# Kernel optimization log

Hardware: AMD Instinct MI355X
Metric: run time of the kernel (lower is better)

## Reference

```python
import jax, jax.numpy as jnp
import numpy as np

# dims: batch, encoder frames, encoder dim, pred-net hidden, joint dim, vocab (blank = V)
B, T, ENC, H, J, V = 32, 64, 1024, 320, 320, 1024
BLANK = V
MAXSYM = 2            # max_symbols_per_step
S = T * MAXSYM        # upper bound on loop-labels iterations (<= MAXSYM steps per frame due to force-blank)


def setup_inputs() -> dict:
    key = jax.random.key(0)
    ks = jax.random.split(key, 10)
    s = 0.05
    return {
        "x": jax.random.normal(ks[0], (B, T, ENC), jnp.float32),
        "out_len": jax.random.randint(ks[1], (B,), T // 2, T + 1, dtype=jnp.int32),
        "W_enc": jax.random.normal(ks[2], (ENC, J), jnp.float32) * s,
        "b_enc": jnp.zeros((J,), jnp.float32),
        "Emb": jax.random.normal(ks[3], (V, H), jnp.float32) * s,
        "W_ih": jax.random.normal(ks[4], (H, 4 * H), jnp.float32) * s,
        "W_hh": jax.random.normal(ks[5], (H, 4 * H), jnp.float32) * s,
        "b_lstm": jnp.zeros((4 * H,), jnp.float32),
        "W_pred": jax.random.normal(ks[6], (H, J), jnp.float32) * s,
        "b_pred": jnp.zeros((J,), jnp.float32),
        "W_out": jax.random.normal(ks[7], (J, V + 1), jnp.float32) * s,
        "b_out": jnp.zeros((V + 1,), jnp.float32),
    }


def _lstm_step(emb, h, c, W_ih, W_hh, b):
    g = emb @ W_ih + h @ W_hh + b
    i, f, gg, o = jnp.split(g, 4, axis=-1)
    c2 = jax.nn.sigmoid(f) * c + jax.nn.sigmoid(i) * jnp.tanh(gg)
    h2 = jax.nn.sigmoid(o) * jnp.tanh(c2)
    return h2, c2


def reference(x, out_len, W_enc, b_enc, Emb, W_ih, W_hh, b_lstm, W_pred, b_pred, W_out, b_out):
    # project_encoder once (as in the torch module)
    x_proj = x @ W_enc + b_enc                      # [B, T, J]
    # SOS step: zero embedding, zero LSTM state (decoder.predict(None, None))
    z = jnp.zeros((B, H), x.dtype)
    h0, c0 = _lstm_step(z, z, z, W_ih, W_hh, b_lstm)
    dec0 = h0 @ W_pred + b_pred                     # project_prednet

    def step(carry, _):
        time, symbols, h, c, dec = carry
        enc_t = jnp.take_along_axis(x_proj, time[:, None, None].astype(jnp.int32), axis=1)[:, 0]  # [B, J]
        logits = jax.nn.relu(enc_t + dec) @ W_out + b_out  # joint_after_projection, [B, V+1]
        scores = logits.max(-1)
        labels = jnp.argmax(logits, -1)
        active = time < out_len
        emit = active & (labels != BLANK)
        # prediction-network step for elements that emitted a non-blank label
        emb = Emb[jnp.where(emit, labels, 0)]
        h2, c2 = _lstm_step(emb, h, c, W_ih, W_hh, b_lstm)
        dec2 = h2 @ W_pred + b_pred
        m = emit[:, None]
        h = jnp.where(m, h2, h)
        c = jnp.where(m, c2, c)
        dec = jnp.where(m, dec2, dec)
        sym2 = jnp.where(emit, symbols + 1, jnp.zeros_like(symbols))
        force = emit & (sym2 >= MAXSYM)             # force blank after max_symbols on one frame
        advance = (active & ~emit) | force          # blank (or forced blank) advances time
        time2 = time + advance.astype(time.dtype)
        sym2 = jnp.where(advance, jnp.zeros_like(sym2), sym2)
        out = (jnp.where(emit, labels, BLANK).astype(jnp.int32),
               jnp.where(active, scores, jnp.zeros_like(scores)),
               time.astype(jnp.int32),
               emit)
        return (time2, sym2, h, c, dec), out

    init = (jnp.zeros((B,), jnp.int32), jnp.zeros((B,), jnp.int32), h0, c0, dec0)
    _, (lab, sc, tm, em) = jax.lax.scan(step, init, None, length=S)
    lengths = em.astype(jnp.int32).sum(0)
    # lab/sc/tm: [S, B] alignment-style records (BLANK filler when nothing emitted);
    # lengths: number of emitted (non-blank) labels per utterance -> equals batched_hyps contents.
    return lab, sc, tm, lengths
```

## Files before the change

kernel.cpp:

```cpp
#include <hip/hip_runtime.h>
#include <math.h>

typedef unsigned long long ull;

constexpr int Bn = 32, Tn = 64, Hn = 320, Jn = 320, Vn = 1024, Sn = 128;
constexpr int G4n = 1280, VP1 = 1025, WO4S = 1028;

constexpr int OFF_XP  = 0;
constexpr int OFF_G   = OFF_XP + Bn*Tn*Jn;
constexpr int OFF_WO4 = OFF_G + Vn*G4n;
constexpr int OFF_WH4 = OFF_WO4 + 80*WO4S*4;
constexpr int OFF_WP4 = OFF_WH4 + 80*G4n*4;
constexpr int OFF_CB  = OFF_WP4 + 80*Jn*4;
constexpr int OFF_DEC = OFF_CB + 2*Bn*Hn;
constexpr int OFF_GB  = OFF_DEC + 2*Bn*Jn;
constexpr int OFF_PB  = OFF_GB + 2*Bn*G4n;
constexpr int OFF_REC = OFF_PB + 2*Bn*8*1028;

__device__ __forceinline__ float sigmf(float x) { return 1.0f / (1.0f + expf(-x)); }

__device__ __forceinline__ ull pack_key(float v, int idx) {
    unsigned u = __float_as_uint(v);
    u = (u & 0x80000000u) ? ~u : (u | 0x80000000u);
    return ((ull)u << 32) | (unsigned)(0x7FFFFFFF - idx);
}
__device__ __forceinline__ float key_val(ull k) {
    unsigned u = (unsigned)(k >> 32);
    return __uint_as_float((u & 0x80000000u) ? (u & 0x7FFFFFFFu) : ~u);
}
__device__ __forceinline__ int key_idx(ull k) { return 0x7FFFFFFF - (int)(k & 0xFFFFFFFFu); }

__device__ __forceinline__ void gemm_tile128(const float* __restrict__ A,
                                             const float* __restrict__ Bm,
                                             const float* __restrict__ bias,
                                             float* __restrict__ C,
                                             int N, int K, int bx, int by,
                                             float (*As)[132], float (*Bs)[65]) {
    const int tx = threadIdx.x & 15, ty = threadIdx.x >> 4;
    const int n0 = bx * 64, m0 = by * 128;
    float acc[8][4] = {};
    for (int k0 = 0; k0 < K; k0 += 16) {
        for (int i = threadIdx.x; i < 2048; i += 256) {
            int mm = i >> 4, kk = i & 15;
            As[kk][mm] = A[(size_t)(m0 + mm) * K + k0 + kk];
        }
        for (int i = threadIdx.x; i < 1024; i += 256) {
            int kk2 = i >> 6, nn = i & 63;
            Bs[kk2][nn] = Bm[(size_t)(k0 + kk2) * N + n0 + nn];
        }
        __syncthreads();
#pragma unroll
        for (int kk = 0; kk < 16; ++kk) {
            float av[8], bv[4];
#pragma unroll
            for (int r = 0; r < 8; ++r) av[r] = As[kk][ty * 8 + r];
#pragma unroll
            for (int r = 0; r < 4; ++r) bv[r] = Bs[kk][tx * 4 + r];
#pragma unroll
            for (int i2 = 0; i2 < 8; ++i2)
#pragma unroll
                for (int j2 = 0; j2 < 4; ++j2) acc[i2][j2] += av[i2] * bv[j2];
        }
        __syncthreads();
    }
#pragma unroll
    for (int i2 = 0; i2 < 8; ++i2)
#pragma unroll
        for (int j2 = 0; j2 < 4; ++j2)
            C[(size_t)(m0 + ty * 8 + i2) * N + n0 + tx * 4 + j2] =
                acc[i2][j2] + bias[n0 + tx * 4 + j2];
}

__global__ __launch_bounds__(256) void preamble(
    const float* __restrict__ x, const float* __restrict__ W_enc,
    const float* __restrict__ b_enc, const float* __restrict__ Emb,
    const float* __restrict__ W_ih, const float* __restrict__ b_lstm,
    const float* __restrict__ W_hh, const float* __restrict__ W_pred,
    const float* __restrict__ W_out,
    float* __restrict__ xp, float* __restrict__ Gm,
    float* __restrict__ Wo4, float* __restrict__ Wh4, float* __restrict__ Wp4) {
    __shared__ float As[16][132];
    __shared__ float Bs[16][65];
    const int blk = blockIdx.x;
    if (blk < 80) {
        gemm_tile128(x, W_enc, b_enc, xp, Jn, 1024, blk % 5, blk / 5, As, Bs);
    } else if (blk < 240) {
        const int t = blk - 80;
        gemm_tile128(Emb, W_ih, b_lstm, Gm, G4n, Hn, t % 20, t / 20, As, Bs);
    } else if (blk < 320) {
        const int k4 = blk - 240;
        for (int c = threadIdx.x; c < VP1; c += 256) {
            float4 v;
            v.x = W_out[(k4 * 4 + 0) * VP1 + c];
            v.y = W_out[(k4 * 4 + 1) * VP1 + c];
            v.z = W_out[(k4 * 4 + 2) * VP1 + c];
            v.w = W_out[(k4 * 4 + 3) * VP1 + c];
            ((float4*)Wo4)[(size_t)k4 * WO4S + c] = v;
        }
    } else if (blk < 400) {
        const int k4 = blk - 320;
        for (int c = threadIdx.x; c < G4n; c += 256) {
            float4 v;
            v.x = W_hh[(k4 * 4 + 0) * G4n + c];
            v.y = W_hh[(k4 * 4 + 1) * G4n + c];
            v.z = W_hh[(k4 * 4 + 2) * G4n + c];
            v.w = W_hh[(k4 * 4 + 3) * G4n + c];
            ((float4*)Wh4)[(size_t)k4 * G4n + c] = v;
        }
    } else {
        const int k4 = blk - 400;
        for (int c = threadIdx.x; c < Jn; c += 256) {
            float4 v;
            v.x = W_pred[(k4 * 4 + 0) * Jn + c];
            v.y = W_pred[(k4 * 4 + 1) * Jn + c];
            v.z = W_pred[(k4 * 4 + 2) * Jn + c];
            v.w = W_pred[(k4 * 4 + 3) * Jn + c];
            ((float4*)Wp4)[(size_t)k4 * Jn + c] = v;
        }
    }
}

__global__ __launch_bounds__(320, 1) void rnnt_step(
    const float* __restrict__ xp, const float* __restrict__ Gm,
    const float* __restrict__ Wo4, const float* __restrict__ Wh4,
    const float* __restrict__ Wp4,
    const float* __restrict__ b_out, const float* __restrict__ b_lstm,
    const float* __restrict__ b_pred, const int* __restrict__ out_len,
    float* __restrict__ cb, float* __restrict__ db, float* __restrict__ gb,
    float* __restrict__ pb, int* __restrict__ rec, float* __restrict__ out,
    int L) {
    __shared__ __align__(16) float h_s[Hn];
    __shared__ __align__(16) float f_s[48];
    __shared__ float dec_s[40];
    __shared__ ull wk_s[5];

    const int w = blockIdx.x, tid = threadIdx.x;
    const int b = w & 31, m = w >> 5;
    const int ol = out_len[b];
    const float4* Wo4f = (const float4*)Wo4;
    const float4* Wh4f = (const float4*)Wh4;
    const float4* Wp4f = (const float4*)Wp4;
    const float4* h4 = (const float4*)h_s;

    int tnew, genN;
    bool doDec;
    if (L == 0) {
        float c0 = sigmf(b_lstm[tid]) * tanhf(b_lstm[2 * Hn + tid]);
        float h0 = sigmf(b_lstm[3 * Hn + tid]) * tanhf(c0);
        h_s[tid] = h0;
        int lc = tid - m * 40;
        if (lc >= 0 && lc < 40) cb[b * Hn + tid] = c0;
        if (m == 0 && tid == 0) {
            int* rn = rec + b * 4;
            rn[0] = 0; rn[1] = 0; rn[2] = 0;
        }
        tnew = 0; genN = 0; doDec = true;
        __syncthreads();
    } else {
        const int* rp = rec + ((L - 1) & 1) * Bn * 4 + b * 4;
        const int told = rp[0], sold = rp[1], len = rp[2];
        if (told >= ol) {
            if (m == 0 && tid == 0) {
                out[(L - 1) * Bn + b] = 1024.0f;
                out[Sn * Bn + (L - 1) * Bn + b] = 0.0f;
                out[2 * Sn * Bn + (L - 1) * Bn + b] = (float)told;
                int* rn = rec + (L & 1) * Bn * 4 + b * 4;
                rn[0] = told; rn[1] = 0; rn[2] = len;
                if (L == Sn) out[3 * Sn * Bn + b] = (float)len;
            }
            return;
        }
        const float* gq = gb + (size_t)((len & 1) * Bn + b) * G4n;
        const float* cv = cb + (size_t)((len & 1) * Bn + b) * Hn;
        float g0 = gq[tid], g1 = gq[Hn + tid], g2 = gq[2 * Hn + tid], g3 = gq[3 * Hn + tid];
        float crv = cv[tid];
        asm volatile("" ::: "memory");
        const float4* pp4 = (const float4*)(pb + (size_t)(((L - 1) & 1) * Bn + b) * 8 * 1028);
        ull key = 0;
        if (tid < 257) {
            float4 sv = make_float4(0.f, 0.f, 0.f, 0.f);
#pragma unroll
            for (int mm = 0; mm < 8; ++mm) {
                float4 v = pp4[mm * 257 + tid];
                sv.x += v.x; sv.y += v.y; sv.z += v.z; sv.w += v.w;
            }
            const int c0 = tid * 4;
            key = pack_key(sv.x + b_out[c0], c0);
            if (c0 + 1 < VP1) { ull k2 = pack_key(sv.y + b_out[c0 + 1], c0 + 1); if (k2 > key) key = k2; }
            if (c0 + 2 < VP1) { ull k2 = pack_key(sv.z + b_out[c0 + 2], c0 + 2); if (k2 > key) key = k2; }
            if (c0 + 3 < VP1) { ull k2 = pack_key(sv.w + b_out[c0 + 3], c0 + 3); if (k2 > key) key = k2; }
        }
#pragma unroll
        for (int d = 1; d < 64; d <<= 1) {
            ull o = __shfl_xor(key, d, 64);
            if (o > key) key = o;
        }
        if ((tid & 63) == 0) wk_s[tid >> 6] = key;
        __syncthreads();
        ull bk = wk_s[0];
#pragma unroll
        for (int i = 1; i < 5; ++i) if (wk_s[i] > bk) bk = wk_s[i];
        const int label = key_idx(bk);
        const bool emit = (label != Vn);
        int sym2 = emit ? sold + 1 : 0;
        const bool force = emit && (sym2 >= 2);
        const bool advance = (!emit) || force;
        tnew = told + (advance ? 1 : 0);
        sym2 = advance ? 0 : sym2;
        const int newlen = len + (emit ? 1 : 0);
        if (m == 0 && tid == 0) {
            out[(L - 1) * Bn + b] = emit ? (float)label : 1024.0f;
            out[Sn * Bn + (L - 1) * Bn + b] = key_val(bk);
            out[2 * Sn * Bn + (L - 1) * Bn + b] = (float)told;
            int* rn = rec + (L & 1) * Bn * 4 + b * 4;
            rn[0] = tnew; rn[1] = sym2; rn[2] = newlen;
            if (L == Sn) out[3 * Sn * Bn + b] = (float)newlen;
        }
        if (L == Sn) return;
        if (tnew >= ol) return;
        genN = newlen;
        doDec = emit;
        if (emit) {
            const float* gE = Gm + (size_t)label * G4n;
            float xi = g0 + gE[tid];
            float xf = g1 + gE[Hn + tid];
            float xg = g2 + gE[2 * Hn + tid];
            float xo = g3 + gE[3 * Hn + tid];
            float c2 = sigmf(xf) * crv + sigmf(xi) * tanhf(xg);
            float h2 = sigmf(xo) * tanhf(c2);
            h_s[tid] = h2;
            int lc = tid - m * 40;
            if (lc >= 0 && lc < 40)
                cb[(size_t)((newlen & 1) * Bn + b) * Hn + tid] = c2;
        } else {
            if (tid < 40)
                dec_s[tid] = db[(size_t)((len & 1) * Bn + b) * Jn + m * 40 + tid];
        }
        __syncthreads();
    }
    if (doDec) {
        if (tid < 160) {
            const int c = m * 160 + tid;
            float ax = 0.f, ay = 0.f, az = 0.f, aw = 0.f;
#pragma unroll 20
            for (int k4 = 0; k4 < 80; ++k4) {
                float4 wv = Wh4f[(size_t)k4 * G4n + c];
                float4 hv = h4[k4];
                ax += wv.x * hv.x; ay += wv.y * hv.y;
                az += wv.z * hv.z; aw += wv.w * hv.w;
            }
            gb[(size_t)((genN & 1) * Bn + b) * G4n + c] = ax + ay + az + aw;
        } else if (tid < 200) {
            const int lc = tid - 160;
            const int c = m * 40 + lc;
            float ax = 0.f, ay = 0.f, az = 0.f, aw = 0.f;
#pragma unroll 20
            for (int k4 = 0; k4 < 80; ++k4) {
                float4 wv = Wp4f[(size_t)k4 * Jn + c];
                float4 hv = h4[k4];
                ax += wv.x * hv.x; ay += wv.y * hv.y;
                az += wv.z * hv.z; aw += wv.w * hv.w;
            }
            float d = b_pred[c] + ax + ay + az + aw;
            dec_s[lc] = d;
            db[(size_t)((genN & 1) * Bn + b) * Jn + c] = d;
        }
        __syncthreads();
    }
    if (tid < 40) {
        const int tc = tnew < (Tn - 1) ? tnew : (Tn - 1);
        f_s[tid] = fmaxf(xp[(size_t)(b * Tn + tc) * Jn + m * 40 + tid] + dec_s[tid], 0.0f);
    }
    __syncthreads();
    {
        const float4* f4 = (const float4*)f_s;
        float4 fr[10];
#pragma unroll
        for (int j = 0; j < 10; ++j) fr[j] = f4[j];
        float* pw = pb + (size_t)((L & 1) * Bn + b) * 8 * 1028 + m * 1028;
        for (int c = tid; c < VP1; c += 320) {
            float ax = 0.f, ay = 0.f, az = 0.f, aw = 0.f;
#pragma unroll
            for (int j = 0; j < 10; ++j) {
                float4 wv = Wo4f[(size_t)(10 * m + j) * WO4S + c];
                float4 fv = fr[j];
                ax += wv.x * fv.x; ay += wv.y * fv.y;
                az += wv.z * fv.z; aw += wv.w * fv.w;
            }
            pw[c] = ax + ay + az + aw;
        }
    }
}

extern "C" void kernel_launch(void* const* d_in, const int* in_sizes, int n_in,
                              void* d_out, int out_size, void* d_ws, size_t ws_size,
                              hipStream_t stream) {
    (void)in_sizes; (void)n_in; (void)out_size; (void)ws_size;
    const float* x      = (const float*)d_in[0];
    const int*   outlen = (const int*)d_in[1];
    const float* W_enc  = (const float*)d_in[2];
    const float* b_enc  = (const float*)d_in[3];
    const float* Emb    = (const float*)d_in[4];
    const float* W_ih   = (const float*)d_in[5];
    const float* W_hh   = (const float*)d_in[6];
    const float* b_lstm = (const float*)d_in[7];
    const float* W_pred = (const float*)d_in[8];
    const float* b_pred = (const float*)d_in[9];
    const float* W_out  = (const float*)d_in[10];
    const float* b_out  = (const float*)d_in[11];

    float* ws  = (float*)d_ws;
    float* xp  = ws + OFF_XP;
    float* Gm  = ws + OFF_G;
    float* Wo4 = ws + OFF_WO4;
    float* Wh4 = ws + OFF_WH4;
    float* Wp4 = ws + OFF_WP4;
    float* cb  = ws + OFF_CB;
    float* db  = ws + OFF_DEC;
    float* gb  = ws + OFF_GB;
    float* pb  = ws + OFF_PB;
    int*   rec = (int*)(ws + OFF_REC);

    preamble<<<480, 256, 0, stream>>>(x, W_enc, b_enc, Emb, W_ih, b_lstm,
                                      W_hh, W_pred, W_out,
                                      xp, Gm, Wo4, Wh4, Wp4);

    for (int L = 0; L <= Sn; ++L)
        rnnt_step<<<256, 320, 0, stream>>>(xp, Gm, Wo4, Wh4, Wp4,
                                           b_out, b_lstm, b_pred, outlen,
                                           cb, db, gb, pb, rec,
                                           (float*)d_out, L);
}
```

Before: 1.996 ms.

## Split decoder GEMV K-dimension across threads and retile preamble GEMMs to 64x64

The preamble GEMMs move from 128x64 tiles with K-step 16 to 64x64 tiles with K-step 32 and float4 global loads. This doubles the block count to 720 for better CU coverage on the one-off projections. In the per-step kernel, the LSTM recurrent GEMV now uses all 320 threads, with two threads per output column each covering half of K and combining through a shuffle. The prediction projection GEMV uses 160 threads, four per output column, reduced with shuffles. This shortens the serial dependency chain of each step's GEMVs at the cost of extra shuffles and more threads contending for weight loads.

```diff
diff --git a/kernel.cpp b/kernel.cpp
--- a/kernel.cpp
+++ b/kernel.cpp
@@ -30,44 +30,45 @@
 }
 __device__ __forceinline__ int key_idx(ull k) { return 0x7FFFFFFF - (int)(k & 0xFFFFFFFFu); }
 
-__device__ __forceinline__ void gemm_tile128(const float* __restrict__ A,
-                                             const float* __restrict__ Bm,
-                                             const float* __restrict__ bias,
-                                             float* __restrict__ C,
-                                             int N, int K, int bx, int by,
-                                             float (*As)[132], float (*Bs)[65]) {
+__device__ __forceinline__ void gemm_tile(const float* __restrict__ A,
+                                          const float* __restrict__ Bm,
+                                          const float* __restrict__ bias,
+                                          float* __restrict__ C,
+                                          int N, int K, int bx, int by,
+                                          float (*As)[73], float (*Bs)[68]) {
     const int tx = threadIdx.x & 15, ty = threadIdx.x >> 4;
-    const int n0 = bx * 64, m0 = by * 128;
-    float acc[8][4] = {};
-    for (int k0 = 0; k0 < K; k0 += 16) {
-        for (int i = threadIdx.x; i < 2048; i += 256) {
-            int mm = i >> 4, kk = i & 15;
-            As[kk][mm] = A[(size_t)(m0 + mm) * K + k0 + kk];
-        }
-        for (int i = threadIdx.x; i < 1024; i += 256) {
-            int kk2 = i >> 6, nn = i & 63;
-            Bs[kk2][nn] = Bm[(size_t)(k0 + kk2) * N + n0 + nn];
-        }
-        __syncthreads();
-#pragma unroll
-        for (int kk = 0; kk < 16; ++kk) {
-            float av[8], bv[4];
-#pragma unroll
-            for (int r = 0; r < 8; ++r) av[r] = As[kk][ty * 8 + r];
-#pragma unroll
-            for (int r = 0; r < 4; ++r) bv[r] = Bs[kk][tx * 4 + r];
-#pragma unroll
-            for (int i2 = 0; i2 < 8; ++i2)
+    const int n0 = bx * 64, m0 = by * 64;
+    float acc[4][4] = {};
+    for (int k0 = 0; k0 < K; k0 += 32) {
+        for (int i = threadIdx.x; i < 512; i += 256) {
+            const int mm = i >> 3, kq = (i & 7) << 2;
+            float4 v = *(const float4*)(A + (size_t)(m0 + mm) * K + k0 + kq);
+            As[kq][mm] = v.x; As[kq + 1][mm] = v.y;
+            As[kq + 2][mm] = v.z; As[kq + 3][mm] = v.w;
+        }
+        for (int i = threadIdx.x; i < 512; i += 256) {
+            const int kk = i >> 4, q = (i & 15) << 2;
+            float4 v = *(const float4*)(Bm + (size_t)(k0 + kk) * N + n0 + q);
+            *(float4*)&Bs[kk][q] = v;
+        }
+        __syncthreads();
+#pragma unroll
+        for (int kk = 0; kk < 32; ++kk) {
+            float av[4], bv[4];
+#pragma unroll
+            for (int r = 0; r < 4; ++r) { av[r] = As[kk][ty * 4 + r]; bv[r] = Bs[kk][tx * 4 + r]; }
+#pragma unroll
+            for (int i2 = 0; i2 < 4; ++i2)
 #pragma unroll
                 for (int j2 = 0; j2 < 4; ++j2) acc[i2][j2] += av[i2] * bv[j2];
         }
         __syncthreads();
     }
 #pragma unroll
-    for (int i2 = 0; i2 < 8; ++i2)
+    for (int i2 = 0; i2 < 4; ++i2)
 #pragma unroll
         for (int j2 = 0; j2 < 4; ++j2)
-            C[(size_t)(m0 + ty * 8 + i2) * N + n0 + tx * 4 + j2] =
+            C[(size_t)(m0 + ty * 4 + i2) * N + n0 + tx * 4 + j2] =
                 acc[i2][j2] + bias[n0 + tx * 4 + j2];
 }
 
@@ -79,16 +80,16 @@
     const float* __restrict__ W_out,
     float* __restrict__ xp, float* __restrict__ Gm,
     float* __restrict__ Wo4, float* __restrict__ Wh4, float* __restrict__ Wp4) {
-    __shared__ float As[16][132];
-    __shared__ float Bs[16][65];
+    __shared__ float As[32][73];
+    __shared__ float Bs[32][68];
     const int blk = blockIdx.x;
-    if (blk < 80) {
-        gemm_tile128(x, W_enc, b_enc, xp, Jn, 1024, blk % 5, blk / 5, As, Bs);
-    } else if (blk < 240) {
-        const int t = blk - 80;
-        gemm_tile128(Emb, W_ih, b_lstm, Gm, G4n, Hn, t % 20, t / 20, As, Bs);
-    } else if (blk < 320) {
-        const int k4 = blk - 240;
+    if (blk < 160) {
+        gemm_tile(x, W_enc, b_enc, xp, Jn, 1024, blk % 5, blk / 5, As, Bs);
+    } else if (blk < 480) {
+        const int t = blk - 160;
+        gemm_tile(Emb, W_ih, b_lstm, Gm, G4n, Hn, t % 20, t / 20, As, Bs);
+    } else if (blk < 560) {
+        const int k4 = blk - 480;
         for (int c = threadIdx.x; c < VP1; c += 256) {
             float4 v;
             v.x = W_out[(k4 * 4 + 0) * VP1 + c];
@@ -97,8 +98,8 @@
             v.w = W_out[(k4 * 4 + 3) * VP1 + c];
             ((float4*)Wo4)[(size_t)k4 * WO4S + c] = v;
         }
-    } else if (blk < 400) {
-        const int k4 = blk - 320;
+    } else if (blk < 640) {
+        const int k4 = blk - 560;
         for (int c = threadIdx.x; c < G4n; c += 256) {
             float4 v;
             v.x = W_hh[(k4 * 4 + 0) * G4n + c];
@@ -108,7 +109,7 @@
             ((float4*)Wh4)[(size_t)k4 * G4n + c] = v;
         }
     } else {
-        const int k4 = blk - 400;
+        const int k4 = blk - 640;
         for (int c = threadIdx.x; c < Jn; c += 256) {
             float4 v;
             v.x = W_pred[(k4 * 4 + 0) * Jn + c];
@@ -239,31 +240,41 @@
         __syncthreads();
     }
     if (doDec) {
-        if (tid < 160) {
-            const int c = m * 160 + tid;
+        {
+            const int cl = tid >> 1, kh = tid & 1;
+            const int c = m * 160 + cl;
             float ax = 0.f, ay = 0.f, az = 0.f, aw = 0.f;
 #pragma unroll 20
-            for (int k4 = 0; k4 < 80; ++k4) {
+            for (int k4 = kh * 40; k4 < kh * 40 + 40; ++k4) {
                 float4 wv = Wh4f[(size_t)k4 * G4n + c];
                 float4 hv = h4[k4];
                 ax += wv.x * hv.x; ay += wv.y * hv.y;
                 az += wv.z * hv.z; aw += wv.w * hv.w;
             }
-            gb[(size_t)((genN & 1) * Bn + b) * G4n + c] = ax + ay + az + aw;
-        } else if (tid < 200) {
-            const int lc = tid - 160;
-            const int c = m * 40 + lc;
+            float part = ax + ay + az + aw;
+            part += __shfl_xor(part, 1, 64);
+            if (kh == 0)
+                gb[(size_t)((genN & 1) * Bn + b) * G4n + c] = part;
+        }
+        if (tid < 160) {
+            const int sc = tid >> 2, kk2 = tid & 3;
+            const int c = m * 40 + sc;
             float ax = 0.f, ay = 0.f, az = 0.f, aw = 0.f;
 #pragma unroll 20
-            for (int k4 = 0; k4 < 80; ++k4) {
+            for (int k4 = kk2 * 20; k4 < kk2 * 20 + 20; ++k4) {
                 float4 wv = Wp4f[(size_t)k4 * Jn + c];
                 float4 hv = h4[k4];
                 ax += wv.x * hv.x; ay += wv.y * hv.y;
                 az += wv.z * hv.z; aw += wv.w * hv.w;
             }
-            float d = b_pred[c] + ax + ay + az + aw;
-            dec_s[lc] = d;
-            db[(size_t)((genN & 1) * Bn + b) * Jn + c] = d;
+            float part = ax + ay + az + aw;
+            part += __shfl_xor(part, 1, 64);
+            part += __shfl_xor(part, 2, 64);
+            if (kk2 == 0) {
+                float d = part + b_pred[c];
+                dec_s[sc] = d;
+                db[(size_t)((genN & 1) * Bn + b) * Jn + c] = d;
+            }
         }
         __syncthreads();
     }
@@ -321,7 +332,7 @@
     float* pb  = ws + OFF_PB;
     int*   rec = (int*)(ws + OFF_REC);
 
-    preamble<<<480, 256, 0, stream>>>(x, W_enc, b_enc, Emb, W_ih, b_lstm,
+    preamble<<<720, 256, 0, stream>>>(x, W_enc, b_enc, Emb, W_ih, b_lstm,
                                       W_hh, W_pred, W_out,
                                       xp, Gm, Wo4, Wh4, Wp4);
 
```

Result: no change. 2.001 ms (+0.2%).
